# Kernel tuning notes

Measured on AMD Instinct MI355X. Metric: run time of the kernel, lower is better.

The kernel has to match this reference:

```python
import jax, jax.numpy as jnp
import numpy as np

HIDDEN = 256
GAMMA = 0.96875
SCALE_BASE = 512


def _rotate_every_two(x):
    x1 = x[..., ::2]
    x2 = x[..., 1::2]
    return jnp.stack((-x2, x1), axis=-1).reshape(x.shape)


def _xpos(x, downscale):
    # x: [B, H, L, D]; offset=0 path of XPOS._forward_impl
    L = x.shape[2]
    D = x.shape[-1]
    half = D // 2
    # buffer: (arange(0, D, 2) + 0.4*D) / (1.4*D)  -> [half]
    scale_vec = (jnp.arange(0, D, 2, dtype=jnp.float32) + 0.4 * D) / (1.4 * D)
    # scale ** (arange(L)/scale_base)[:, None] -> [L, half]
    exps = jnp.arange(L, dtype=jnp.float32) / SCALE_BASE
    scale = scale_vec[None, :] ** exps[:, None]
    # fixed_pos_embedding on scale (dim = half)
    inv_freq = 1.0 / (10000.0 ** (jnp.arange(half, dtype=jnp.float32) / half))
    sinusoid = jnp.arange(L, dtype=jnp.float32)[:, None] * inv_freq[None, :]  # [L, half]
    sin = jnp.sin(sinusoid)
    cos = jnp.cos(sinusoid)
    if downscale:
        scale = 1.0 / scale
    sin2 = jnp.repeat(sin * scale, 2, axis=-1)  # duplicate_interleave -> [L, D]
    cos2 = jnp.repeat(cos * scale, 2, axis=-1)
    return x * cos2 + _rotate_every_two(x) * sin2


def _decay_mask(L):
    n = jnp.arange(L)[:, None]
    m = jnp.arange(L)[None, :]
    return jnp.where(n >= m, jnp.power(GAMMA, (n - m).astype(jnp.float32)), 0.0)


def setup_inputs() -> dict:
    key = jax.random.key(0)
    k1, k2, k3, k4 = jax.random.split(key, 4)
    B, H, L, D = 8, 4, 2048, HIDDEN
    X = jax.random.normal(k1, (B, H, L, D), dtype=jnp.float32)
    W_Q = jax.random.normal(k2, (D, D), dtype=jnp.float32) / D
    W_K = jax.random.normal(k3, (D, D), dtype=jnp.float32) / D
    W_V = jax.random.normal(k4, (D, D), dtype=jnp.float32) / D
    return {"X": X, "W_Q": W_Q, "W_K": W_K, "W_V": W_V}


def reference(X, W_Q, W_K, W_V):
    L = X.shape[2]
    Q = X @ W_Q
    K = X @ W_K
    Q = _xpos(Q, downscale=False)
    K = _xpos(K, downscale=True)
    V = X @ W_V
    D = _decay_mask(L)  # [L, L]
    att = jnp.einsum('bhnd,bhmd->bhnm', Q, K) * D[None, None]
    return att @ V
```

## Files before the change

### kernel.cpp

```cpp
#include <hip/hip_runtime.h>
#include <stdint.h>

typedef unsigned short u16;
typedef unsigned int   u32;
typedef __attribute__((ext_vector_type(8))) short  bf16x8;
typedef __attribute__((ext_vector_type(4))) float  f32x4;
typedef __attribute__((ext_vector_type(4))) u32    u32x4;
typedef __attribute__((ext_vector_type(2))) u32    u32x2;

#define L_SEQ 2048
#define DMODEL 256

__device__ __forceinline__ u16 f2bf(float x){
  u32 u = __float_as_uint(x);
  return (u16)((u + 0x7FFFu + ((u >> 16) & 1u)) >> 16);
}

__device__ __forceinline__ u32 pack2(float a, float b){
  return (u32)f2bf(a) | ((u32)f2bf(b) << 16);
}

__device__ __forceinline__ void gload_lds16(const void* g, void* l){
  __builtin_amdgcn_global_load_lds(
      (const __attribute__((address_space(1))) u32*)g,
      (__attribute__((address_space(3))) u32*)l, 16, 0, 0);
}

__global__ __launch_bounds__(256) void k_prep(
    const float* __restrict__ X,
    const float* __restrict__ wq, const float* __restrict__ wk,
    const float* __restrict__ wv,
    float2* __restrict__ tq2, float2* __restrict__ tk2,
    u16* __restrict__ wt2, u16* __restrict__ Xb2)
{
  const int bid = blockIdx.x;
  const int tid = threadIdx.x;
  if (bid < 1024){
    int idx = bid * 256 + tid;
    int n = idx >> 7, hi = idx & 127;
    float fn = (float)n, fi = (float)hi;
    float invf = exp2f(-(fi * (1.0f/128.0f)) * 13.2877124f);
    float ang = fn * invf;
    float s = sinf(ang), c = cosf(ang);
    float sv = (2.0f * fi + 102.4f) * (1.0f / 358.4f);
    float sc = exp2f((fn * (1.0f/512.0f)) * log2f(sv));
    float2 q; q.x = c * sc;  q.y = s * sc;
    tq2[idx] = q;
    float inv = 1.0f / sc;
    float2 k; k.x = c * inv; k.y = s * inv;
    tk2[idx] = k;
  } else if (bid < 1120){
    int idx = (bid - 1024) * 256 + tid;
    int kc = idx / 6144, r = idx % 6144;
    int col = r >> 3, p = r & 7;
    int j = p ^ (col & 7);
    int wsel = col >> 8, c = col & 255;
    const float* src = (wsel == 0) ? wq : ((wsel == 1) ? wk : wv);
    int k0 = kc * 64 + j * 8;
    u32x4 v;
    v.x = pack2(src[(k0+0)*256 + c], src[(k0+1)*256 + c]);
    v.y = pack2(src[(k0+2)*256 + c], src[(k0+3)*256 + c]);
    v.z = pack2(src[(k0+4)*256 + c], src[(k0+5)*256 + c]);
    v.w = pack2(src[(k0+6)*256 + c], src[(k0+7)*256 + c]);
    *(u32x4*)(wt2 + (size_t)idx * 8) = v;
  } else {
    int idx = (bid - 1120) * 256 + tid;
    int row = idx >> 5, g = idx & 31;
    int kc = g >> 3, j = g & 7;
    int p = j ^ (row & 7);
    const float4* src = (const float4*)(X + (size_t)row * 256 + g * 8);
    float4 a = src[0], b = src[1];
    u32x4 v;
    v.x = pack2(a.x, a.y); v.y = pack2(a.z, a.w);
    v.z = pack2(b.x, b.y); v.w = pack2(b.z, b.w);
    *(u32x4*)(Xb2 + (((size_t)kc * 65536 + row) * 8 + p) * 8) = v;
  }
}

__global__ __launch_bounds__(256, 2) void k_proj(
    const u16* __restrict__ Xb2, const u16* __restrict__ Wt2,
    const float2* __restrict__ tq2, const float2* __restrict__ tk2,
    u16* __restrict__ Qx, u16* __restrict__ Kx, u16* __restrict__ VT)
{
  __shared__ char smem[65536];
  const int p0 = blockIdx.x;
  const int l = (p0 & 7) * 384 + (p0 >> 3);
  const int ct = l % 6;
  const int rt = l / 6;
  const int wsel = ct >> 1;
  const int mcol0 = (ct & 1) * 128;
  const int row0 = rt * 128;
  const int bh = rt >> 4;
  const int tid = threadIdx.x;
  const int lane = tid & 63, wid = tid >> 6;
  const int h = lane >> 4, l15 = lane & 15;
  const int wrg = wid >> 1, wcg = wid & 1;

  f32x4 acc[4][4] = {};

  auto stage = [&](int kc, int buf){
    const u16* xsrc = Xb2 + ((size_t)kc * 65536 + row0) * 64;
    const u16* wsrc = Wt2 + ((size_t)kc * 768 + ct * 128) * 64;
    char* xdst = smem + buf * 16384;
    char* wdst = smem + 32768 + buf * 16384;
#pragma unroll
    for (int t = 0; t < 4; ++t){
      int ci = t * 256 + tid;
      gload_lds16(xsrc + ci * 8, xdst + (t * 256 + wid * 64) * 16);
      gload_lds16(wsrc + ci * 8, wdst + (t * 256 + wid * 64) * 16);
    }
  };

  stage(0, 0);
  __syncthreads();

  for (int kc = 0; kc < 4; ++kc){
    const int cur = kc & 1;
    if (kc < 3) stage(kc + 1, cur ^ 1);

    const char* lX = smem + cur * 16384;
    const char* lW = smem + 32768 + cur * 16384;
#pragma unroll
    for (int kb = 0; kb < 2; ++kb){
      bf16x8 xf[4], wf[4];
#pragma unroll
      for (int b = 0; b < 4; ++b){
        int r = wrg * 64 + b * 16 + l15;
        int p = (kb * 4 + h) ^ (r & 7);
        xf[b] = *(const bf16x8*)(lX + r * 128 + p * 16);
      }
#pragma unroll
      for (int a = 0; a < 4; ++a){
        int c = wcg * 64 + a * 16 + l15;
        int p = (kb * 4 + h) ^ (c & 7);
        wf[a] = *(const bf16x8*)(lW + c * 128 + p * 16);
      }
      if (wsel < 2){
#pragma unroll
        for (int a = 0; a < 4; ++a)
#pragma unroll
          for (int b = 0; b < 4; ++b)
            acc[a][b] = __builtin_amdgcn_mfma_f32_16x16x32_bf16(
                wf[a], xf[b], acc[a][b], 0, 0, 0);
      } else {
#pragma unroll
        for (int b = 0; b < 4; ++b)
#pragma unroll
          for (int a = 0; a < 4; ++a)
            acc[b][a] = __builtin_amdgcn_mfma_f32_16x16x32_bf16(
                xf[b], wf[a], acc[b][a], 0, 0, 0);
      }
    }
    __syncthreads();
  }

  if (wsel < 2){
    const float2* tt = (wsel == 0) ? tq2 : tk2;
    u16* Od = (wsel == 0) ? Qx : Kx;
#pragma unroll
    for (int a = 0; a < 4; ++a){
      int d0 = mcol0 + wcg * 64 + a * 16 + h * 4;
#pragma unroll
      for (int b = 0; b < 4; ++b){
        int n = row0 + wrg * 64 + b * 16 + l15;
        int pos = n & 2047;
        f32x4 v = acc[a][b];
        float4 t = *(const float4*)(tt + pos * 128 + (d0 >> 1));
        float y0 = v.x * t.x - v.y * t.y;
        float y1 = v.y * t.x + v.x * t.y;
        float y2 = v.z * t.z - v.w * t.w;
        float y3 = v.w * t.z + v.z * t.w;
        u32x2 p2; p2.x = pack2(y0, y1); p2.y = pack2(y2, y3);
        int lrow = wrg * 64 + b * 16 + l15;
        int lcolb = (wcg * 64 + a * 16 + h * 4) * 2;
        *(u32x2*)(smem + lrow * 256 + (lcolb ^ ((lrow & 7) << 4))) = p2;
      }
    }
    __syncthreads();
    {
      const int r = tid >> 1;
      const int cbase = (tid & 1) * 8;
      u16* orow = Od + (size_t)(row0 + r) * 256 + mcol0 + cbase * 8;
#pragma unroll
      for (int j = 0; j < 8; ++j){
        int c16 = cbase + j;
        u32x4 v = *(const u32x4*)(smem + r * 256 +
                                  ((c16 * 16) ^ ((r & 7) << 4)));
        *(u32x4*)(orow + j * 8) = v;
      }
    }
  } else {
#pragma unroll
    for (int b = 0; b < 4; ++b){
      int lpos = wrg * 64 + b * 16 + h * 4;
#pragma unroll
      for (int a = 0; a < 4; ++a){
        int ld = wcg * 64 + a * 16 + l15;
        f32x4 v = acc[b][a];
        u32x2 p2; p2.x = pack2(v.x, v.y); p2.y = pack2(v.z, v.w);
        *(u32x2*)(smem + ld * 256 + ((lpos * 2) ^ ((ld & 7) << 4))) = p2;
      }
    }
    __syncthreads();
    {
      const int dloc = tid >> 1;
      const int cbase = (tid & 1) * 8;
      const int posbase = (rt & 15) * 128;
      u16* orow = VT + ((size_t)bh * DMODEL + mcol0 + dloc) * 2048 +
                  posbase + cbase * 8;
#pragma unroll
      for (int j = 0; j < 8; ++j){
        int c16 = cbase + j;
        u32x4 v = *(const u32x4*)(smem + dloc * 256 +
                                  ((c16 * 16) ^ ((dloc & 7) << 4)));
        *(u32x4*)(orow + j * 8) = v;
      }
    }
  }
}

__global__ __launch_bounds__(512) void k_attn(
    const u16* __restrict__ Qx, const u16* __restrict__ Kx,
    const u16* __restrict__ VT, float* __restrict__ out)
{
  __shared__ char smem[131072];

  const int pbid = blockIdx.x;
  const int bid = ((pbid & 7) << 6) | (pbid >> 3);
  const int bh = bid >> 4, i = bid & 15;
  const int tid = threadIdx.x;
  const int lane = tid & 63, w = tid >> 6;
  const int h = lane >> 4, l15 = lane & 15;
  const int n_g = i * 128 + w * 16 + l15;

  bf16x8 q[8];
  const u16* qbase = Qx + ((size_t)bh * 2048 + n_g) * 256;
#pragma unroll
  for (int kb = 0; kb < 8; ++kb)
    q[kb] = *(const bf16x8*)(qbase + kb * 32 + h * 8);

  f32x4 ot[16] = {};

  int j_lo = 2 * i - 2; if (j_lo < 0) j_lo = 0;
  const int j_hi = 2 * i + 1;
  const float L2G = -0.04580369f;
  const float GI1 = 1.03225806f;
  const float GI2 = 1.06555671f;
  const float GI3 = 1.09993040f;

  auto stage = [&](int j, int buf){
    const u16* kbase = Kx + ((size_t)bh * 2048 + j * 64) * 256;
    char* kdst = smem + buf * 32768;
#pragma unroll
    for (int t = 0; t < 4; ++t){
      int s = (w * 4 + t) * 64 + lane;
      int m = s >> 5, c = s & 31;
      gload_lds16(kbase + m * 256 + ((c ^ (m & 7)) * 8),
                  kdst + (w * 4 + t) * 1024);
    }
    const u16* vbase = VT + (size_t)bh * (DMODEL * 2048) + j * 64;
    char* vdst = smem + 65536 + buf * 32768;
#pragma unroll
    for (int t = 0; t < 4; ++t){
      int s = (w * 4 + t) * 64 + lane;
      int d = s >> 3, c = s & 7;
      gload_lds16(vbase + (size_t)d * 2048 + ((c ^ (d & 7)) * 8),
                  vdst + (w * 4 + t) * 1024);
    }
  };

  stage(j_lo, 0);
  __syncthreads();

  for (int j = j_lo; j <= j_hi; ++j){
    const int cur = (j - j_lo) & 1;
    if (j < j_hi) stage(j + 1, cur ^ 1);

    if (i * 128 + w * 16 + 15 >= j * 64){
      const char* ldsK = smem + cur * 32768;
      const char* ldsV = smem + 65536 + cur * 32768;
      f32x4 sacc[4] = {};
      __builtin_amdgcn_s_setprio(1);
#pragma unroll
      for (int kb = 0; kb < 8; ++kb){
#pragma unroll
        for (int mt = 0; mt < 4; ++mt){
          int m = mt * 16 + l15;
          int chunk = kb * 4 + h;
          bf16x8 a = *(const bf16x8*)(ldsK + m * 512 +
                                      ((chunk ^ (m & 7)) * 16));
          sacc[mt] = __builtin_amdgcn_mfma_f32_16x16x32_bf16(
              a, q[kb], sacc[mt], 0, 0, 0);
        }
      }
      __builtin_amdgcn_s_setprio(0);
      u32 dA[4], dB[4];
#pragma unroll
      for (int mt = 0; mt < 4; ++mt){
        int m0 = j * 64 + mt * 16 + h * 4;
        int dl = n_g - m0;
        float base = exp2f((float)dl * L2G);
        float v0 = (dl     >= 0) ? sacc[mt].x * base       : 0.0f;
        float v1 = (dl - 1 >= 0) ? sacc[mt].y * base * GI1 : 0.0f;
        float v2 = (dl - 2 >= 0) ? sacc[mt].z * base * GI2 : 0.0f;
        float v3 = (dl - 3 >= 0) ? sacc[mt].w * base * GI3 : 0.0f;
        dA[mt] = pack2(v0, v1);
        dB[mt] = pack2(v2, v3);
      }
      int s0 = l15 + 32 * (h & 1);
      int s1 = s0 + 16;
      bool lo = (h < 2);
#pragma unroll
      for (int kt = 0; kt < 2; ++kt){
        u32 a0 = (u32)__shfl((int)dA[2 * kt],     s0, 64);
        u32 a1 = (u32)__shfl((int)dA[2 * kt + 1], s0, 64);
        u32 b0 = (u32)__shfl((int)dB[2 * kt],     s0, 64);
        u32 b1 = (u32)__shfl((int)dB[2 * kt + 1], s0, 64);
        u32 a2 = (u32)__shfl((int)dA[2 * kt],     s1, 64);
        u32 a3 = (u32)__shfl((int)dA[2 * kt + 1], s1, 64);
        u32 b2 = (u32)__shfl((int)dB[2 * kt],     s1, 64);
        u32 b3 = (u32)__shfl((int)dB[2 * kt + 1], s1, 64);
        union { u32 u[4]; bf16x8 v; } uu;
        uu.u[0] = lo ? a0 : a1;
        uu.u[1] = lo ? b0 : b1;
        uu.u[2] = lo ? a2 : a3;
        uu.u[3] = lo ? b2 : b3;
        bf16x8 bfrag = uu.v;
        __builtin_amdgcn_s_setprio(1);
#pragma unroll
        for (int dt = 0; dt < 16; ++dt){
          int d = dt * 16 + l15;
          int chunk = kt * 4 + h;
          bf16x8 a = *(const bf16x8*)(ldsV + d * 128 +
                                      ((chunk ^ (d & 7)) * 16));
          ot[dt] = __builtin_amdgcn_mfma_f32_16x16x32_bf16(
              a, bfrag, ot[dt], 0, 0, 0);
        }
        __builtin_amdgcn_s_setprio(0);
      }
    }
    __syncthreads();
  }

  float* obase = out + ((size_t)bh * 2048 + n_g) * 256;
#pragma unroll
  for (int dt = 0; dt < 16; ++dt)
    *(f32x4*)(obase + dt * 16 + h * 4) = ot[dt];
}

extern "C" void kernel_launch(void* const* d_in, const int* in_sizes, int n_in,
                              void* d_out, int out_size, void* d_ws, size_t ws_size,
                              hipStream_t stream)
{
  (void)in_sizes; (void)n_in; (void)out_size; (void)ws_size;
  const float* X  = (const float*)d_in[0];
  const float* WQ = (const float*)d_in[1];
  const float* WK = (const float*)d_in[2];
  const float* WV = (const float*)d_in[3];
  float* out = (float*)d_out;

  char* ws = (char*)d_ws;
  float2* tq2 = (float2*)ws;
  float2* tk2 = (float2*)(ws + (2u << 20));
  u16* wt2 = (u16*)(ws + (4u << 20));
  u16* qx = (u16*)(ws + 4718592);
  u16* kx = (u16*)(ws + 38273024);
  u16* vt = (u16*)(ws + 71827456);

  u16* xb2 = (u16*)d_out;

  k_prep<<<dim3(9312), dim3(256), 0, stream>>>(X, WQ, WK, WV,
                                               tq2, tk2, wt2, xb2);
  k_proj<<<dim3(3072), dim3(256), 0, stream>>>(xb2, wt2, tq2, tk2, qx, kx, vt);
  k_attn<<<dim3(512), dim3(512), 0, stream>>>(qx, kx, vt, out);
}
```

Before: 126.5 us.

## Fuse Q projection and xPos rotation into attention kernel prologue

Removes the Q projection from the projection kernel and computes each block's 128-row Q tile inside the attention kernel using MFMA, applying the xPos rotation and keeping Q in shared memory. The goal is to avoid writing Q to global memory and reading it back, and to shrink the projection grid. In exchange, the attention kernel gains an unpipelined prologue with extra syncs. Because the output buffer is no longer scratch space, the bf16 X copy now lives in the workspace region that used to hold Q.

New measurement: 125.9 us. No clear change (-0.5%).

```diff
diff --git a/kernel.cpp b/kernel.cpp
--- a/kernel.cpp
+++ b/kernel.cpp
@@ -79,14 +79,14 @@
 
 __global__ __launch_bounds__(256, 2) void k_proj(
     const u16* __restrict__ Xb2, const u16* __restrict__ Wt2,
-    const float2* __restrict__ tq2, const float2* __restrict__ tk2,
-    u16* __restrict__ Qx, u16* __restrict__ Kx, u16* __restrict__ VT)
+    const float2* __restrict__ tk2,
+    u16* __restrict__ Kx, u16* __restrict__ VT)
 {
   __shared__ char smem[65536];
   const int p0 = blockIdx.x;
-  const int l = (p0 & 7) * 384 + (p0 >> 3);
-  const int ct = l % 6;
-  const int rt = l / 6;
+  const int l = (p0 & 7) * 256 + (p0 >> 3);
+  const int ct = l & 3;
+  const int rt = l >> 2;
   const int wsel = ct >> 1;
   const int mcol0 = (ct & 1) * 128;
   const int row0 = rt * 128;
@@ -100,7 +100,7 @@
 
   auto stage = [&](int kc, int buf){
     const u16* xsrc = Xb2 + ((size_t)kc * 65536 + row0) * 64;
-    const u16* wsrc = Wt2 + ((size_t)kc * 768 + ct * 128) * 64;
+    const u16* wsrc = Wt2 + ((size_t)kc * 768 + 256 + ct * 128) * 64;
     char* xdst = smem + buf * 16384;
     char* wdst = smem + 32768 + buf * 16384;
 #pragma unroll
@@ -135,7 +135,7 @@
         int p = (kb * 4 + h) ^ (c & 7);
         wf[a] = *(const bf16x8*)(lW + c * 128 + p * 16);
       }
-      if (wsel < 2){
+      if (wsel == 0){
 #pragma unroll
         for (int a = 0; a < 4; ++a)
 #pragma unroll
@@ -154,9 +154,8 @@
     __syncthreads();
   }
 
-  if (wsel < 2){
-    const float2* tt = (wsel == 0) ? tq2 : tk2;
-    u16* Od = (wsel == 0) ? Qx : Kx;
+  if (wsel == 0){
+    u16* Od = Kx;
 #pragma unroll
     for (int a = 0; a < 4; ++a){
       int d0 = mcol0 + wcg * 64 + a * 16 + h * 4;
@@ -165,7 +164,7 @@
         int n = row0 + wrg * 64 + b * 16 + l15;
         int pos = n & 2047;
         f32x4 v = acc[a][b];
-        float4 t = *(const float4*)(tt + pos * 128 + (d0 >> 1));
+        float4 t = *(const float4*)(tk2 + pos * 128 + (d0 >> 1));
         float y0 = v.x * t.x - v.y * t.y;
         float y1 = v.y * t.x + v.x * t.y;
         float y2 = v.z * t.z - v.w * t.w;
@@ -220,8 +219,10 @@
 }
 
 __global__ __launch_bounds__(512) void k_attn(
-    const u16* __restrict__ Qx, const u16* __restrict__ Kx,
-    const u16* __restrict__ VT, float* __restrict__ out)
+    const u16* __restrict__ Xb2, const u16* __restrict__ Wt2,
+    const float2* __restrict__ tq2,
+    const u16* __restrict__ Kx, const u16* __restrict__ VT,
+    float* __restrict__ out)
 {
   __shared__ char smem[131072];
 
@@ -232,12 +233,83 @@
   const int lane = tid & 63, w = tid >> 6;
   const int h = lane >> 4, l15 = lane & 15;
   const int n_g = i * 128 + w * 16 + l15;
+  const int row0q = bid * 128;
+
+  {
+    const int wrgQ = w >> 2, wcgQ = w & 3;
+    f32x4 qacc[4][4] = {};
+    char* xbuf = smem;
+    char* wbuf = smem + 16384;
+    for (int kc = 0; kc < 4; ++kc){
+      const u16* xsrc = Xb2 + ((size_t)kc * 65536 + row0q) * 64;
+      const u16* wsrc = Wt2 + ((size_t)kc * 768) * 64;
+#pragma unroll
+      for (int t = 0; t < 2; ++t){
+        int ci = (w * 2 + t) * 64 + lane;
+        gload_lds16(xsrc + ci * 8, xbuf + (w * 2 + t) * 1024);
+      }
+#pragma unroll
+      for (int t = 0; t < 4; ++t){
+        int ci = (w * 4 + t) * 64 + lane;
+        gload_lds16(wsrc + ci * 8, wbuf + (w * 4 + t) * 1024);
+      }
+      __syncthreads();
+#pragma unroll
+      for (int kb = 0; kb < 2; ++kb){
+        bf16x8 xf[4], wf[4];
+#pragma unroll
+        for (int b = 0; b < 4; ++b){
+          int r = wrgQ * 64 + b * 16 + l15;
+          int p = (kb * 4 + h) ^ (r & 7);
+          xf[b] = *(const bf16x8*)(xbuf + r * 128 + p * 16);
+        }
+#pragma unroll
+        for (int a = 0; a < 4; ++a){
+          int c = wcgQ * 64 + a * 16 + l15;
+          int p = (kb * 4 + h) ^ (c & 7);
+          wf[a] = *(const bf16x8*)(wbuf + c * 128 + p * 16);
+        }
+#pragma unroll
+        for (int a = 0; a < 4; ++a)
+#pragma unroll
+          for (int b = 0; b < 4; ++b)
+            qacc[a][b] = __builtin_amdgcn_mfma_f32_16x16x32_bf16(
+                wf[a], xf[b], qacc[a][b], 0, 0, 0);
+      }
+      __syncthreads();
+    }
+    char* qt = smem + 65536;
+#pragma unroll
+    for (int a = 0; a < 4; ++a){
+      int d0 = wcgQ * 64 + a * 16 + h * 4;
+#pragma unroll
+      for (int b = 0; b < 4; ++b){
+        int lrow = wrgQ * 64 + b * 16 + l15;
+        int pos = (row0q + lrow) & 2047;
+        f32x4 v = qacc[a][b];
+        float4 t = *(const float4*)(tq2 + pos * 128 + (d0 >> 1));
+        float y0 = v.x * t.x - v.y * t.y;
+        float y1 = v.y * t.x + v.x * t.y;
+        float y2 = v.z * t.z - v.w * t.w;
+        float y3 = v.w * t.z + v.z * t.w;
+        u32x2 p2; p2.x = pack2(y0, y1); p2.y = pack2(y2, y3);
+        *(u32x2*)(qt + lrow * 512 + ((d0 * 2) ^ ((lrow & 7) << 4))) = p2;
+      }
+    }
+    __syncthreads();
+  }
 
   bf16x8 q[8];
-  const u16* qbase = Qx + ((size_t)bh * 2048 + n_g) * 256;
-#pragma unroll
-  for (int kb = 0; kb < 8; ++kb)
-    q[kb] = *(const bf16x8*)(qbase + kb * 32 + h * 8);
+  {
+    const char* qt = smem + 65536;
+    int r = w * 16 + l15;
+#pragma unroll
+    for (int kb = 0; kb < 8; ++kb){
+      int off = (kb * 64 + h * 16) ^ ((r & 7) << 4);
+      q[kb] = *(const bf16x8*)(qt + r * 512 + off);
+    }
+  }
+  __syncthreads();
 
   f32x4 ot[16] = {};
 
@@ -363,14 +435,12 @@
   float2* tq2 = (float2*)ws;
   float2* tk2 = (float2*)(ws + (2u << 20));
   u16* wt2 = (u16*)(ws + (4u << 20));
-  u16* qx = (u16*)(ws + 4718592);
+  u16* xb2 = (u16*)(ws + 4718592);
   u16* kx = (u16*)(ws + 38273024);
   u16* vt = (u16*)(ws + 71827456);
 
-  u16* xb2 = (u16*)d_out;
-
   k_prep<<<dim3(9312), dim3(256), 0, stream>>>(X, WQ, WK, WV,
                                                tq2, tk2, wt2, xb2);
-  k_proj<<<dim3(3072), dim3(256), 0, stream>>>(xb2, wt2, tq2, tk2, qx, kx, vt);
-  k_attn<<<dim3(512), dim3(512), 0, stream>>>(qx, kx, vt, out);
-}
+  k_proj<<<dim3(2048), dim3(256), 0, stream>>>(xb2, wt2, tk2, kx, vt);
+  k_attn<<<dim3(512), dim3(512), 0, stream>>>(xb2, wt2, tq2, kx, vt, out);
+}
```
